# Performance work log

Measured on AMD Instinct MI355X. Metric: run time of the kernel, lower is better.

Reference implementation:

```python
import jax, jax.numpy as jnp
import numpy as np
from jax import lax

INPUT_DIM = 2048
OUTPUT_DIM = 2048
BATCH = 256
T = 20.0
DT = 0.5
TAU_M = 20.0
TAU_S = 5.0
STEPS = int(T / DT)  # 40


def setup_inputs() -> dict:
    key = jax.random.key(0)
    k1, k2 = jax.random.split(key)
    # spike times on the t = i*dt grid (exactly representable in fp32)
    steps_idx = jax.random.randint(k1, (BATCH, INPUT_DIM), 0, STEPS)
    inp = steps_idx.astype(jnp.float32) * DT
    # nn.init.normal_(weight, mean=0.1, std=0.1)
    weight = 0.1 + 0.1 * jax.random.normal(k2, (OUTPUT_DIM, INPUT_DIM), dtype=jnp.float32)
    return {"input": inp, "weight": weight}


def _manual_forward(inp, weight):
    B = inp.shape[0]
    O = weight.shape[0]
    V0 = jnp.zeros((B, O), dtype=weight.dtype)
    I0 = jnp.zeros((B, O), dtype=weight.dtype)  # I[-1] row is zero at i=0

    def step(carry, i):
        V, I_prev = carry
        t = i.astype(weight.dtype) * DT
        V = V + (DT / TAU_M) * (I_prev - V)
        spikes_in = (inp == t).astype(weight.dtype)            # [B, in]
        I_i = (1.0 - DT / TAU_S) * I_prev + spikes_in @ weight.T  # [B, out]
        s = (V > 1.0).astype(weight.dtype)
        V = (1.0 - s) * V
        return (V, I_i), (I_i, s)

    (_, _), (I, post_spikes) = lax.scan(step, (V0, I0), jnp.arange(STEPS))
    # first spike time: idx decreasing so argmax picks earliest spiking step
    idx = jnp.arange(STEPS, 0, -1, dtype=weight.dtype)[:, None, None]
    first = jnp.argmax(idx * post_spikes, axis=0).astype(jnp.float32)
    # neurons with no spike (or spike at step 0, faithful to original) -> T
    first = jnp.where(first == 0.0, jnp.float32(T), first)
    return first, I, post_spikes


def reference(input, weight):
    first_post_spikes, _, _ = _manual_forward(input, weight)
    return first_post_spikes
```

## Files before the change

kernel.cpp:

```cpp
#include <hip/hip_runtime.h>


#define IN_DIM     2048
#define OUT_DIM    2048
#define BATCH      256
#define STEPS      40
#define NSLICE     8
#define ORD_STRIDE 2304

__global__ __launch_bounds__(256) void transpose_k(const float* __restrict__ W,
                                                   float* __restrict__ WT) {
    __shared__ float tile[64][65];
    const int bx = blockIdx.x;
    const int by = blockIdx.y;
    const int x  = threadIdx.x & 63;
    const int y4 = threadIdx.x >> 6;
#pragma unroll
    for (int i = 0; i < 16; ++i) {
        const int a = y4 * 16 + i;
        tile[a][x] = W[(size_t)(by * 64 + a) * IN_DIM + (bx * 64 + x)];
    }
    if (bx == 0 && y4 == 0)
        WT[(size_t)IN_DIM * OUT_DIM + by * 64 + x] = 0.0f;
    __syncthreads();
#pragma unroll
    for (int i = 0; i < 16; ++i) {
        const int r = y4 * 16 + i;
        WT[(size_t)(bx * 64 + r) * OUT_DIM + (by * 64 + x)] = tile[x][r];
    }
}

__global__ __launch_bounds__(256) void sort_k(const float* __restrict__ inp,
                                              int* __restrict__ ord,
                                              int* __restrict__ offs) {
    __shared__ int hist[256 * STEPS];
    __shared__ int tot[STEPS];
    __shared__ int binstart[STEPS + 1];
    const int b = blockIdx.x, t = threadIdx.x;
    for (int i = t; i < 256 * STEPS; i += 256) hist[i] = 0;
    __syncthreads();
    int ks[8];
#pragma unroll
    for (int i = 0; i < 8; ++i) {
        const float v = inp[b * IN_DIM + t * 8 + i];
        const int k = (int)(v * 2.0f);
        ks[i] = k;
        ++hist[t * STEPS + k];
    }
    __syncthreads();
    if (t < STEPS) {
        int run = 0;
        for (int tt = 0; tt < 256; ++tt) {
            const int c = hist[tt * STEPS + t];
            hist[tt * STEPS + t] = run;
            run += c;
        }
        tot[t] = run;
    }
    __syncthreads();
    if (t == 0) {
        int run = 0;
        for (int k = 0; k < STEPS; ++k) {
            binstart[k] = run;
            run += (tot[k] + 3) & ~3;
        }
        binstart[STEPS] = run;
    }
    __syncthreads();
    if (t <= STEPS) offs[b * (STEPS + 1) + t] = binstart[t];
#pragma unroll
    for (int i = 0; i < 8; ++i) {
        const int k = ks[i];
        const int pos = binstart[k] + hist[t * STEPS + k]++;
        ord[b * ORD_STRIDE + pos] = (t * 8 + i) * (OUT_DIM * 4);
    }
    if (t < STEPS) {
        const int beg = binstart[t] + tot[t];
        const int end = binstart[t] + ((tot[t] + 3) & ~3);
        for (int p = beg; p < end; ++p)
            ord[b * ORD_STRIDE + p] = IN_DIM * (OUT_DIM * 4);
    }
}

__global__ __launch_bounds__(64) void snn_k(const float* __restrict__ WT,
                                            const int* __restrict__ ord,
                                            const int* __restrict__ offs,
                                            float* __restrict__ out) {
    const int wid  = blockIdx.x;
    const int s    = wid & (NSLICE - 1);
    const int b    = wid >> 3;
    const int lane = threadIdx.x;
    const char* wbase = (const char*)WT + ((s * 256 + lane * 4) << 2);
    const int* __restrict__ ob  = ord  + b * ORD_STRIDE;
    const int* __restrict__ off = offs + b * (STEPS + 1);

    float I0 = 0.f, I1 = 0.f, I2 = 0.f, I3 = 0.f;
    float V0 = 0.f, V1 = 0.f, V2 = 0.f, V3 = 0.f;
    int   f0 = 0,   f1 = 0,   f2 = 0,   f3 = 0;
    int p = 0;
    for (int k = 0; k < STEPS; ++k) {
        const int e = off[k + 1];
        float a0 = 0.f, a1 = 0.f, a2 = 0.f, a3 = 0.f;
        for (; p < e; p += 4) {
            const int4 jj = *(const int4*)(ob + p);
            const float4 w0 = *(const float4*)(wbase + jj.x);
            const float4 w1 = *(const float4*)(wbase + jj.y);
            const float4 w2 = *(const float4*)(wbase + jj.z);
            const float4 w3 = *(const float4*)(wbase + jj.w);
            a0 += w0.x; a1 += w0.y; a2 += w0.z; a3 += w0.w;
            a0 += w1.x; a1 += w1.y; a2 += w1.z; a3 += w1.w;
            a0 += w2.x; a1 += w2.y; a2 += w2.z; a3 += w2.w;
            a0 += w3.x; a1 += w3.y; a2 += w3.z; a3 += w3.w;
        }
        V0 += 0.025f * (I0 - V0);
        V1 += 0.025f * (I1 - V1);
        V2 += 0.025f * (I2 - V2);
        V3 += 0.025f * (I3 - V3);
        I0 = 0.9f * I0 + a0;
        I1 = 0.9f * I1 + a1;
        I2 = 0.9f * I2 + a2;
        I3 = 0.9f * I3 + a3;
        if (V0 > 1.0f) { if (f0 == 0) f0 = k; V0 = 0.f; }
        if (V1 > 1.0f) { if (f1 == 0) f1 = k; V1 = 0.f; }
        if (V2 > 1.0f) { if (f2 == 0) f2 = k; V2 = 0.f; }
        if (V3 > 1.0f) { if (f3 == 0) f3 = k; V3 = 0.f; }
        if (__all((f0 != 0) & (f1 != 0) & (f2 != 0) & (f3 != 0))) break;
    }
    float4 r;
    r.x = f0 ? (float)f0 : 20.0f;
    r.y = f1 ? (float)f1 : 20.0f;
    r.z = f2 ? (float)f2 : 20.0f;
    r.w = f3 ? (float)f3 : 20.0f;
    *(float4*)(out + (size_t)b * OUT_DIM + s * 256 + lane * 4) = r;
}

extern "C" void kernel_launch(void* const* d_in, const int* in_sizes, int n_in,
                              void* d_out, int out_size, void* d_ws, size_t ws_size,
                              hipStream_t stream) {
    const float* inp = (const float*)d_in[0];
    const float* W   = (const float*)d_in[1];
    float* out = (float*)d_out;
    char*  ws  = (char*)d_ws;

    float* WT = (float*)ws;
    const size_t WT_BYTES = (size_t)(IN_DIM + 1) * OUT_DIM * sizeof(float);
    int* ord  = (int*)(ws + WT_BYTES);
    int* offs = (int*)(ws + WT_BYTES + (size_t)BATCH * ORD_STRIDE * sizeof(int));

    transpose_k<<<dim3(IN_DIM / 64, OUT_DIM / 64), 256, 0, stream>>>(W, WT);
    sort_k<<<BATCH, 256, 0, stream>>>(inp, ord, offs);
    snn_k<<<BATCH * NSLICE, 64, 0, stream>>>(WT, ord, offs, out);
}
```

Baseline: 52.49 us.

## Split output neurons across 32 slices with one neuron per lane

Each lane now handles one output neuron with scalar weight loads instead of four neurons with float4 loads, and the neuron dimension is split into 32 slices instead of 8. This gives four times as many wavefronts, which raises parallelism and occupancy and shortens each wave's serial gather chain. In exchange, every wavefront re-reads the same index list, so index loads grow fourfold, and 4-byte loads fetch less per memory instruction than 16-byte ones.

Result: slower. 53.65 us (+2.2%).

```diff
diff --git a/kernel.cpp b/kernel.cpp
--- a/kernel.cpp
+++ b/kernel.cpp
@@ -5,7 +5,7 @@
 #define OUT_DIM    2048
 #define BATCH      256
 #define STEPS      40
-#define NSLICE     8
+#define NSLICE     32
 #define ORD_STRIDE 2304
 
 __global__ __launch_bounds__(256) void transpose_k(const float* __restrict__ W,
@@ -88,50 +88,31 @@
                                             float* __restrict__ out) {
     const int wid  = blockIdx.x;
     const int s    = wid & (NSLICE - 1);
-    const int b    = wid >> 3;
+    const int b    = wid >> 5;
     const int lane = threadIdx.x;
-    const char* wbase = (const char*)WT + ((s * 256 + lane * 4) << 2);
+    const char* wb = (const char*)(WT + s * 64 + lane);
     const int* __restrict__ ob  = ord  + b * ORD_STRIDE;
     const int* __restrict__ off = offs + b * (STEPS + 1);
 
-    float I0 = 0.f, I1 = 0.f, I2 = 0.f, I3 = 0.f;
-    float V0 = 0.f, V1 = 0.f, V2 = 0.f, V3 = 0.f;
-    int   f0 = 0,   f1 = 0,   f2 = 0,   f3 = 0;
+    float I = 0.f, V = 0.f;
+    int   f = 0;
     int p = 0;
     for (int k = 0; k < STEPS; ++k) {
         const int e = off[k + 1];
-        float a0 = 0.f, a1 = 0.f, a2 = 0.f, a3 = 0.f;
+        float a = 0.f;
         for (; p < e; p += 4) {
             const int4 jj = *(const int4*)(ob + p);
-            const float4 w0 = *(const float4*)(wbase + jj.x);
-            const float4 w1 = *(const float4*)(wbase + jj.y);
-            const float4 w2 = *(const float4*)(wbase + jj.z);
-            const float4 w3 = *(const float4*)(wbase + jj.w);
-            a0 += w0.x; a1 += w0.y; a2 += w0.z; a3 += w0.w;
-            a0 += w1.x; a1 += w1.y; a2 += w1.z; a3 += w1.w;
-            a0 += w2.x; a1 += w2.y; a2 += w2.z; a3 += w2.w;
-            a0 += w3.x; a1 += w3.y; a2 += w3.z; a3 += w3.w;
+            a += *(const float*)(wb + jj.x);
+            a += *(const float*)(wb + jj.y);
+            a += *(const float*)(wb + jj.z);
+            a += *(const float*)(wb + jj.w);
         }
-        V0 += 0.025f * (I0 - V0);
-        V1 += 0.025f * (I1 - V1);
-        V2 += 0.025f * (I2 - V2);
-        V3 += 0.025f * (I3 - V3);
-        I0 = 0.9f * I0 + a0;
-        I1 = 0.9f * I1 + a1;
-        I2 = 0.9f * I2 + a2;
-        I3 = 0.9f * I3 + a3;
-        if (V0 > 1.0f) { if (f0 == 0) f0 = k; V0 = 0.f; }
-        if (V1 > 1.0f) { if (f1 == 0) f1 = k; V1 = 0.f; }
-        if (V2 > 1.0f) { if (f2 == 0) f2 = k; V2 = 0.f; }
-        if (V3 > 1.0f) { if (f3 == 0) f3 = k; V3 = 0.f; }
-        if (__all((f0 != 0) & (f1 != 0) & (f2 != 0) & (f3 != 0))) break;
+        V += 0.025f * (I - V);
+        I = 0.9f * I + a;
+        if (V > 1.0f) { if (f == 0) f = k; V = 0.f; }
+        if (__all(f != 0)) break;
     }
-    float4 r;
-    r.x = f0 ? (float)f0 : 20.0f;
-    r.y = f1 ? (float)f1 : 20.0f;
-    r.z = f2 ? (float)f2 : 20.0f;
-    r.w = f3 ? (float)f3 : 20.0f;
-    *(float4*)(out + (size_t)b * OUT_DIM + s * 256 + lane * 4) = r;
+    out[(size_t)b * OUT_DIM + s * 64 + lane] = f ? (float)f : 20.0f;
 }
 
 extern "C" void kernel_launch(void* const* d_in, const int* in_sizes, int n_in,
```
